# Optimization experiments

Hardware: AMD Instinct MI355X
Metric: run time of the kernel (lower is better)

## Reference

```python
import jax, jax.numpy as jnp
import numpy as np

BATCH = 2048
INPUT_DIM = 256    # == output_units, since Dense output is fed back into the cell
DEC_UNITS = 1024
OUTPUT_STEPS = 96
OUTPUT_UNITS = 256


def setup_inputs() -> dict:
    key = jax.random.key(0)
    ks = jax.random.split(key, 8)
    scale = 0.05
    return {
        "last_input": jax.random.normal(ks[0], (BATCH, INPUT_DIM), dtype=jnp.float32),
        "h0": jax.random.normal(ks[1], (BATCH, DEC_UNITS), dtype=jnp.float32),
        "c0": jax.random.normal(ks[2], (BATCH, DEC_UNITS), dtype=jnp.float32),
        # LSTMCell params (Keras layout: kernel [in, 4*units], recurrent_kernel [units, 4*units], bias [4*units]; gate order i,f,c,o)
        "Wk": jax.random.normal(ks[3], (INPUT_DIM, 4 * DEC_UNITS), dtype=jnp.float32) * scale,
        "Wr": jax.random.normal(ks[4], (DEC_UNITS, 4 * DEC_UNITS), dtype=jnp.float32) * scale,
        "b": jax.random.normal(ks[5], (4 * DEC_UNITS,), dtype=jnp.float32) * scale,
        # Dense output projection
        "Wd": jax.random.normal(ks[6], (DEC_UNITS, OUTPUT_UNITS), dtype=jnp.float32) * scale,
        "bd": jax.random.normal(ks[7], (OUTPUT_UNITS,), dtype=jnp.float32) * scale,
    }


def reference(last_input, h0, c0, Wk, Wr, b, Wd, bd):
    def step(carry, _):
        x, h, c = carry
        # fused gate GEMM: [B, in] @ [in, 4U] + [B, U] @ [U, 4U]
        z = x @ Wk + h @ Wr + b
        zi, zf, zg, zo = jnp.split(z, 4, axis=-1)  # Keras gate order: i, f, c(g), o
        i = jax.nn.sigmoid(zi)
        f = jax.nn.sigmoid(zf)
        o = jax.nn.sigmoid(zo)
        c_new = f * c + i * jnp.tanh(zg)
        h_new = o * jnp.tanh(c_new)
        pred = h_new @ Wd + bd  # fed back as next step's input
        return (pred, h_new, c_new), pred

    _, preds = jax.lax.scan(step, (last_input, h0, c0), None, length=OUTPUT_STEPS)
    # preds: [T, B, out] -> [B, T, out] (matches tf.transpose(predictions, [1,0,2]))
    return jnp.transpose(preds, (1, 0, 2))
```

## Files before the change

### kernel.cpp

```cpp
#include <hip/hip_runtime.h>
#include <hip/hip_bf16.h>
#include <stdint.h>

#define B_SZ 2048
#define U_SZ 1024
#define G_SZ 4096
#define I_SZ 256
#define O_SZ 256
#define T_SZ 96
#define K1_SZ 1280

typedef _Float16 half8 __attribute__((ext_vector_type(8)));
typedef float float4v __attribute__((ext_vector_type(4)));

__device__ inline float sigm_f(float x) { return 1.0f / (1.0f + __expf(-x)); }
__device__ inline float tanh_f(float x) { return 1.0f - 2.0f / (1.0f + __expf(2.0f * x)); }

__device__ inline short f2h(float x) {
    return __builtin_bit_cast(short, (_Float16)x);
}

__device__ inline void cp16(const void* g, void* l) {
    __builtin_amdgcn_global_load_lds(
        (const __attribute__((address_space(1))) void*)g,
        (__attribute__((address_space(3))) void*)l,
        16, 0, 0);
}


__global__ void transpose_reord(const float* __restrict__ in, float* __restrict__ out, int K) {
    __shared__ float s[32][33];
    int c0 = blockIdx.x * 32, k0 = blockIdx.y * 32;
    int tx = threadIdx.x, ty = threadIdx.y;
#pragma unroll
    for (int i = 0; i < 4; i++)
        s[ty + 8 * i][tx] = in[(long)(k0 + ty + 8 * i) * G_SZ + c0 + tx];
    __syncthreads();
#pragma unroll
    for (int i = 0; i < 4; i++) {
        int cc = ty + 8 * i;
        int c = c0 + cc;
        int n = 4 * (c & 1023) + (c >> 10);
        out[(long)n * K + k0 + tx] = s[tx][cc];
    }
}

__global__ void transpose_f32(const float* __restrict__ in, float* __restrict__ out, int R, int C) {
    __shared__ float s[32][33];
    int c0 = blockIdx.x * 32, r0 = blockIdx.y * 32;
    int tx = threadIdx.x, ty = threadIdx.y;
#pragma unroll
    for (int i = 0; i < 4; i++)
        s[ty + 8 * i][tx] = in[(long)(r0 + ty + 8 * i) * C + c0 + tx];
    __syncthreads();
#pragma unroll
    for (int i = 0; i < 4; i++)
        out[(long)(c0 + ty + 8 * i) * R + r0 + tx] = s[tx][ty + 8 * i];
}

__global__ void transpose_f16(const float* __restrict__ in, short* __restrict__ out, int R, int C) {
    __shared__ float s[32][33];
    int c0 = blockIdx.x * 32, r0 = blockIdx.y * 32;
    int tx = threadIdx.x, ty = threadIdx.y;
#pragma unroll
    for (int i = 0; i < 4; i++)
        s[ty + 8 * i][tx] = in[(long)(r0 + ty + 8 * i) * C + c0 + tx];
    __syncthreads();
#pragma unroll
    for (int i = 0; i < 4; i++)
        out[(long)(c0 + ty + 8 * i) * R + r0 + tx] = f2h(s[tx][ty + 8 * i]);
}

__global__ void cast_f16(const float* __restrict__ in, short* __restrict__ out) {
    long i = (long)blockIdx.x * 256 + threadIdx.x;
    out[i] = f2h(in[i]);
}

__global__ void build_b0t(const float* __restrict__ WkT, const float* __restrict__ WrT,
                          short* __restrict__ B0T) {
    long idx = (long)blockIdx.x * 256 + threadIdx.x;
    long n = idx / K1_SZ, k = idx % K1_SZ;
    float v = (k < I_SZ) ? WkT[n * I_SZ + k] : WrT[n * U_SZ + (k - I_SZ)];
    B0T[idx] = f2h(v);
}

__global__ void build_x0(const float* __restrict__ x0, const float* __restrict__ h0,
                         short* __restrict__ X0) {
    long idx = (long)blockIdx.x * 256 + threadIdx.x;
    long m = idx / K1_SZ, k = idx % K1_SZ;
    float v = (k < I_SZ) ? x0[m * I_SZ + k] : h0[m * U_SZ + (k - I_SZ)];
    X0[idx] = f2h(v);
}

__global__ void build_ber(const float* __restrict__ Wk, const float* __restrict__ b,
                          const float* __restrict__ bd, float* __restrict__ beR,
                          float* __restrict__ bR) {
    int c = blockIdx.x * 256 + threadIdx.x;
    float s = 0.0f;
    for (int p = 0; p < I_SZ; p++) s += bd[p] * Wk[(long)p * G_SZ + c];
    int slot = 4 * (c & 1023) + (c >> 10);
    bR[slot] = b[c];
    beR[slot] = b[c] + s;
}

__global__ void zero_ctr(unsigned int* __restrict__ c) { c[threadIdx.x] = 0u; }

__device__ __forceinline__ void gemm_core(char* smem, const char* gA, const char* gB,
                                          long Kb, int KI, int w, int l,
                                          float4v (&acc)[4][4]) {
    const int lr = l & 15, lk = l >> 4;
    const int wg = w >> 1, wb = w & 1;
    char* const lA = smem + (w * 32) * 128;
    char* const lB = smem + 32768 + (w * 16) * 128;

    auto stage = [&](int kt, int b) {
        const long go = (long)kt * 128;
        char* dA = lA + b * 49152;
        char* dB = lB + b * 49152;
#pragma unroll
        for (int ci = 0; ci < 4; ++ci) cp16(gA + (long)ci * 8 * Kb + go, dA + ci * 1024);
#pragma unroll
        for (int ci = 0; ci < 2; ++ci) cp16(gB + (long)ci * 8 * Kb + go, dB + ci * 1024);
    };
    auto compute = [&](int b) {
        const char* As = smem + b * 49152;
        const char* Bs = As + 32768;
#pragma unroll
        for (int ks = 0; ks < 2; ++ks) {
            half8 af[4], bf[4];
            const int chunk = (ks * 4 + lk) ^ (lr & 7);
#pragma unroll
            for (int mi = 0; mi < 4; ++mi)
                af[mi] = *(const half8*)(As + (wg * 64 + mi * 16 + lr) * 128 + chunk * 16);
#pragma unroll
            for (int ni = 0; ni < 4; ++ni)
                bf[ni] = *(const half8*)(Bs + (wb * 64 + ni * 16 + lr) * 128 + chunk * 16);
            __builtin_amdgcn_s_setprio(1);
#pragma unroll
            for (int mi = 0; mi < 4; ++mi)
#pragma unroll
                for (int ni = 0; ni < 4; ++ni)
                    acc[mi][ni] = __builtin_amdgcn_mfma_f32_16x16x32_f16(
                        af[mi], bf[ni], acc[mi][ni], 0, 0, 0);
            __builtin_amdgcn_s_setprio(0);
        }
    };

    stage(0, 0);
    stage(1, 1);
    int bc = 0, bs = 2;
    for (int kt = 0; kt < KI; ++kt) {
        if (kt < KI - 1)
            asm volatile("s_waitcnt vmcnt(6) lgkmcnt(0)" ::: "memory");
        else
            asm volatile("s_waitcnt vmcnt(0) lgkmcnt(0)" ::: "memory");
        __builtin_amdgcn_s_barrier();
        asm volatile("" ::: "memory");
        if (kt + 2 < KI) stage(kt + 2, bs);
        compute(bc);
        bc = (bc == 2) ? 0 : bc + 1;
        bs = (bs == 2) ? 0 : bs + 1;
    }
}

__device__ __forceinline__ void gemm_core_paced(char* smem, const char* gA, const char* gB,
                                                long Kb, int KI, int w, int l,
                                                float4v (&acc)[4][4], int tid, int xcd,
                                                unsigned int* pace, int sync_base) {
    const int lr = l & 15, lk = l >> 4;
    const int wg = w >> 1, wb = w & 1;
    char* const lA = smem + (w * 32) * 128;
    char* const lB = smem + 32768 + (w * 16) * 128;

    auto stage = [&](int kt, int b) {
        const long go = (long)kt * 128;
        char* dA = lA + b * 49152;
        char* dB = lB + b * 49152;
#pragma unroll
        for (int ci = 0; ci < 4; ++ci) cp16(gA + (long)ci * 8 * Kb + go, dA + ci * 1024);
#pragma unroll
        for (int ci = 0; ci < 2; ++ci) cp16(gB + (long)ci * 8 * Kb + go, dB + ci * 1024);
    };
    auto compute = [&](int b) {
        const char* As = smem + b * 49152;
        const char* Bs = As + 32768;
#pragma unroll
        for (int ks = 0; ks < 2; ++ks) {
            half8 af[4], bf[4];
            const int chunk = (ks * 4 + lk) ^ (lr & 7);
#pragma unroll
            for (int mi = 0; mi < 4; ++mi)
                af[mi] = *(const half8*)(As + (wg * 64 + mi * 16 + lr) * 128 + chunk * 16);
#pragma unroll
            for (int ni = 0; ni < 4; ++ni)
                bf[ni] = *(const half8*)(Bs + (wb * 64 + ni * 16 + lr) * 128 + chunk * 16);
            __builtin_amdgcn_s_setprio(1);
#pragma unroll
            for (int mi = 0; mi < 4; ++mi)
#pragma unroll
                for (int ni = 0; ni < 4; ++ni)
                    acc[mi][ni] = __builtin_amdgcn_mfma_f32_16x16x32_f16(
                        af[mi], bf[ni], acc[mi][ni], 0, 0, 0);
            __builtin_amdgcn_s_setprio(0);
        }
    };

    stage(0, 0);
    stage(1, 1);
    int bc = 0, bs = 2;
    for (int kt = 0; kt < KI; ++kt) {
        if ((kt & 3) == 0 && kt != 0) {
            asm volatile("" ::: "memory");
            if (tid == 0) {
                const unsigned int tgt = 32u * (unsigned int)(sync_base + (kt >> 2));
                __hip_atomic_fetch_add(&pace[xcd * 32], 1u, __ATOMIC_RELAXED,
                                       __HIP_MEMORY_SCOPE_AGENT);
                while (__hip_atomic_load(&pace[xcd * 32], __ATOMIC_RELAXED,
                                         __HIP_MEMORY_SCOPE_AGENT) < tgt)
                    __builtin_amdgcn_s_sleep(1);
            }
            __builtin_amdgcn_s_barrier();
            asm volatile("" ::: "memory");
        }
        if (kt < KI - 1)
            asm volatile("s_waitcnt vmcnt(6) lgkmcnt(0)" ::: "memory");
        else
            asm volatile("s_waitcnt vmcnt(0) lgkmcnt(0)" ::: "memory");
        __builtin_amdgcn_s_barrier();
        asm volatile("" ::: "memory");
        if (kt + 2 < KI) stage(kt + 2, bs);
        compute(bc);
        bc = (bc == 2) ? 0 : bc + 1;
        bs = (bs == 2) ? 0 : bs + 1;
    }
}

__global__ __launch_bounds__(512, 2) void lstm_step(
    const short* __restrict__ A, const short* __restrict__ Bm, int K,
    float* __restrict__ cT, const float* __restrict__ beR, short* __restrict__ hOut,
    unsigned int* __restrict__ pace, int sync_base) {
    __shared__ char smem[147456];

    const int tid = threadIdx.x;
    const int w = tid >> 6, l = tid & 63;
    const int wg = w >> 1, wb = w & 1;
    const int bid = blockIdx.x;
    const int xcd = bid & 7, idx = bid >> 3;
    const int n_blk = (xcd & 3) * 4 + (idx & 3);
    const int m_blk = (xcd >> 2) * 8 + (idx >> 2);
    const long Kb = (long)K * 2;

    float4v acc[4][4];
#pragma unroll
    for (int i = 0; i < 4; i++)
#pragma unroll
        for (int j = 0; j < 4; j++) acc[i][j] = (float4v)0.0f;

    const int r8 = l >> 3, s8 = l & 7, gch = s8 ^ r8;
    const char* gA = (const char*)A + ((long)(n_blk * 256 + w * 32 + r8)) * Kb + gch * 16;
    const char* gB = (const char*)Bm + ((long)(m_blk * 128 + w * 16 + r8)) * Kb + gch * 16;

    gemm_core_paced(smem, gA, gB, Kb, K >> 6, w, l, acc, tid, xcd, pace, sync_base);

    const int lr = l & 15, lk = l >> 4;
    short* hs = (short*)smem;
    __syncthreads();
    const int j_base = n_blk * 64 + wg * 16;
    const int m_base = m_blk * 128 + wb * 64;
#pragma unroll
    for (int mi = 0; mi < 4; ++mi) {
        int j = j_base + mi * 4 + lk;
        float4v bias = *(const float4v*)(beR + 4 * j);
#pragma unroll
        for (int ni = 0; ni < 4; ++ni) {
            int m = m_base + ni * 16 + lr;
            float zi = acc[mi][ni][0] + bias[0];
            float zf = acc[mi][ni][1] + bias[1];
            float zg = acc[mi][ni][2] + bias[2];
            float zo = acc[mi][ni][3] + bias[3];
            float ig = sigm_f(zi), fg = sigm_f(zf), gg = tanh_f(zg), og = sigm_f(zo);
            long cidx = (long)j * B_SZ + m;
            float cn = fg * cT[cidx] + ig * gg;
            cT[cidx] = cn;
            float h = og * tanh_f(cn);
            int mm = wb * 64 + ni * 16 + lr;
            int jj = wg * 16 + mi * 4 + lk;
            hs[mm * 64 + (jj ^ ((mm & 7) << 3))] = f2h(h);
        }
    }
    __syncthreads();
    {
        const int q = tid & 7;
        int rr = tid >> 3;
#pragma unroll
        for (int it = 0; it < 2; ++it, rr += 64) {
            uint4 v = *(const uint4*)(hs + rr * 64 + ((q ^ (rr & 7)) * 8));
            *(uint4*)(hOut + (long)(m_blk * 128 + rr) * U_SZ + n_blk * 64 + q * 8) = v;
        }
    }
}

__global__ __launch_bounds__(512, 2) void dense_out(
    const short* __restrict__ Hm, const short* __restrict__ WdT,
    const float* __restrict__ bd, float* __restrict__ out, int t_fix) {
    __shared__ char smem[147456];

    const int tid = threadIdx.x;
    const int w = tid >> 6, l = tid & 63;
    const int wg = w >> 1, wb = w & 1;
    const int o_blk = blockIdx.x, m_blk = blockIdx.y;
    const long Kb = U_SZ * 2;

    float4v acc[4][4];
#pragma unroll
    for (int i = 0; i < 4; i++)
#pragma unroll
        for (int j = 0; j < 4; j++) acc[i][j] = (float4v)0.0f;

    const int r8 = l >> 3, s8 = l & 7, gch = s8 ^ r8;
    const char* gA = (const char*)Hm + ((long)(m_blk * 256 + w * 32 + r8)) * Kb + gch * 16;
    const char* gB = (const char*)WdT + ((long)(o_blk * 128 + w * 16 + r8)) * Kb + gch * 16;

    gemm_core(smem, gA, gB, Kb, U_SZ >> 6, w, l, acc);

    const int lr = l & 15, lk = l >> 4;
#pragma unroll
    for (int ni = 0; ni < 4; ++ni) {
        int o = o_blk * 128 + wb * 64 + ni * 16 + lr;
        float bo = bd[o];
#pragma unroll
        for (int mi = 0; mi < 4; ++mi) {
#pragma unroll
            for (int r = 0; r < 4; ++r) {
                int m = m_blk * 256 + wg * 64 + mi * 16 + lk * 4 + r;
                int t = (t_fix >= 0) ? t_fix : (m >> 11);
                int b = (t_fix >= 0) ? m : (m & 2047);
                out[(long)b * (T_SZ * O_SZ) + (long)t * O_SZ + o] = acc[mi][ni][r] + bo;
            }
        }
    }
}

__global__ __launch_bounds__(512, 2) void fold_mfma(
    const short* __restrict__ WkTh, const short* __restrict__ Wdh,
    const float* __restrict__ WrT, short* __restrict__ WeT) {
    __shared__ char smem[147456];

    const int tid = threadIdx.x;
    const int w = tid >> 6, l = tid & 63;
    const int wg = w >> 1, wb = w & 1;
    const int n_blk = blockIdx.x, k_blk = blockIdx.y;
    const long Kb = I_SZ * 2;

    float4v acc[4][4];
#pragma unroll
    for (int i = 0; i < 4; i++)
#pragma unroll
        for (int j = 0; j < 4; j++) acc[i][j] = (float4v)0.0f;

    const int r8 = l >> 3, s8 = l & 7, gch = s8 ^ r8;
    const char* gA = (const char*)WkTh + ((long)(n_blk * 256 + w * 32 + r8)) * Kb + gch * 16;
    const char* gB = (const char*)Wdh + ((long)(k_blk * 128 + w * 16 + r8)) * Kb + gch * 16;

    gemm_core(smem, gA, gB, Kb, I_SZ >> 6, w, l, acc);

    const int lr = l & 15, lk = l >> 4;
#pragma unroll
    for (int mi = 0; mi < 4; ++mi)
#pragma unroll
        for (int ni = 0; ni < 4; ++ni)
#pragma unroll
            for (int r = 0; r < 4; ++r) {
                long n = n_blk * 256 + wg * 64 + mi * 16 + lk * 4 + r;
                long k = k_blk * 128 + wb * 64 + ni * 16 + lr;
                WeT[n * U_SZ + k] = f2h(WrT[n * U_SZ + k] + acc[mi][ni][r]);
            }
}

extern "C" void kernel_launch(void* const* d_in, const int* in_sizes, int n_in,
                              void* d_out, int out_size, void* d_ws, size_t ws_size,
                              hipStream_t stream) {
    (void)in_sizes; (void)n_in; (void)out_size;
    const float* x0 = (const float*)d_in[0];
    const float* h0 = (const float*)d_in[1];
    const float* c0 = (const float*)d_in[2];
    const float* Wk = (const float*)d_in[3];
    const float* Wr = (const float*)d_in[4];
    const float* bb = (const float*)d_in[5];
    const float* Wd = (const float*)d_in[6];
    const float* bd = (const float*)d_in[7];
    float* out = (float*)d_out;

    char* p = (char*)d_ws;
    auto alloc = [&](size_t bytes) {
        char* r = p;
        p += (bytes + 255) & ~(size_t)255;
        return r;
    };
    short* WeT = (short*)alloc((size_t)G_SZ * U_SZ * 2);
    short* B0T = (short*)alloc((size_t)G_SZ * K1_SZ * 2);
    short* X0 = (short*)alloc((size_t)B_SZ * K1_SZ * 2);
    short* WdT = (short*)alloc((size_t)O_SZ * U_SZ * 2);
    short* WkTh = (short*)alloc((size_t)G_SZ * I_SZ * 2);
    short* Wdh = (short*)alloc((size_t)U_SZ * I_SZ * 2);
    float* beR = (float*)alloc((size_t)U_SZ * 4 * 4);
    float* bR = (float*)alloc((size_t)U_SZ * 4 * 4);
    float* cT = (float*)alloc((size_t)U_SZ * B_SZ * 4);
    unsigned int* pace = (unsigned int*)alloc(1024);
    char* R = p;
    const size_t SLAB = (size_t)B_SZ * U_SZ * 2;
    size_t rem = (ws_size > (size_t)(R - (char*)d_ws)) ? ws_size - (size_t)(R - (char*)d_ws) : 0;
    bool hist = rem >= (size_t)T_SZ * SLAB;

    float* WkT = (float*)R;
    float* WrT = (float*)(R + (size_t)G_SZ * I_SZ * 4);

    zero_ctr<<<1, 256, 0, stream>>>(pace);
    transpose_reord<<<dim3(G_SZ / 32, I_SZ / 32), dim3(32, 8), 0, stream>>>(Wk, WkT, I_SZ);
    transpose_reord<<<dim3(G_SZ / 32, U_SZ / 32), dim3(32, 8), 0, stream>>>(Wr, WrT, U_SZ);
    cast_f16<<<(G_SZ * I_SZ) / 256, 256, 0, stream>>>(WkT, WkTh);
    cast_f16<<<(U_SZ * I_SZ) / 256, 256, 0, stream>>>(Wd, Wdh);
    fold_mfma<<<dim3(G_SZ / 256, U_SZ / 128), 512, 0, stream>>>(WkTh, Wdh, WrT, WeT);
    build_b0t<<<(int)(((size_t)G_SZ * K1_SZ) / 256), 256, 0, stream>>>(WkT, WrT, B0T);
    build_ber<<<G_SZ / 256, 256, 0, stream>>>(Wk, bb, bd, beR, bR);
    transpose_f16<<<dim3(O_SZ / 32, U_SZ / 32), dim3(32, 8), 0, stream>>>(Wd, WdT, U_SZ, O_SZ);
    transpose_f32<<<dim3(U_SZ / 32, B_SZ / 32), dim3(32, 8), 0, stream>>>(c0, cT, B_SZ, U_SZ);
    build_x0<<<(int)(((size_t)B_SZ * K1_SZ) / 256), 256, 0, stream>>>(x0, h0, X0);

    auto slab = [&](int t) -> short* {
        if (hist) return (short*)(R + (size_t)(t - 1) * SLAB);
        return (short*)(R + (size_t)((t - 1) & 1) * SLAB);
    };

    int sb = 0;
    for (int t = 1; t <= T_SZ; ++t) {
        if (t == 1) {
            lstm_step<<<256, 512, 0, stream>>>(
                B0T, X0, K1_SZ, cT, bR, slab(1), pace, sb);
            sb += ((K1_SZ >> 6) - 1) >> 2;
        } else {
            lstm_step<<<256, 512, 0, stream>>>(
                WeT, slab(t - 1), U_SZ, cT, beR, slab(t), pace, sb);
            sb += ((U_SZ >> 6) - 1) >> 2;
        }
        if (!hist)
            dense_out<<<dim3(2, B_SZ / 256), 512, 0, stream>>>(slab(t), WdT, bd, out, t - 1);
    }
    if (hist)
        dense_out<<<dim3(2, (T_SZ * B_SZ) / 256), 512, 0, stream>>>((short*)R, WdT, bd, out, -1);
}
```

Before: 3.021 ms.

## Drop per-XCD atomic pacing in LSTM step; retile dense output GEMM

Removes the cross-block atomic pacing barrier inside the LSTM step GEMM, along with its counter buffer and zeroing kernel, so blocks run unthrottled through the K loop. The dense output projection moves to a new 256-thread, double-buffered GEMM core with 128x128 tiles and a smaller LDS footprint, meant to raise occupancy and grid size. Without pacing, blocks on the same XCD may drift apart and lose the L2 reuse of shared weight tiles that the pacing was meant to keep.

```diff
diff --git a/kernel.cpp b/kernel.cpp
--- a/kernel.cpp
+++ b/kernel.cpp
@@ -102,8 +102,6 @@
     bR[slot] = b[c];
     beR[slot] = b[c] + s;
 }
-
-__global__ void zero_ctr(unsigned int* __restrict__ c) { c[threadIdx.x] = 0u; }
 
 __device__ __forceinline__ void gemm_core(char* smem, const char* gA, const char* gB,
                                           long Kb, int KI, int w, int l,
@@ -163,27 +161,26 @@
     }
 }
 
-__device__ __forceinline__ void gemm_core_paced(char* smem, const char* gA, const char* gB,
-                                                long Kb, int KI, int w, int l,
-                                                float4v (&acc)[4][4], int tid, int xcd,
-                                                unsigned int* pace, int sync_base) {
+__device__ __forceinline__ void gemm_core4(char* smem, const char* gA, const char* gB,
+                                           long Kb, int KI, int w, int l,
+                                           float4v (&acc)[4][4]) {
     const int lr = l & 15, lk = l >> 4;
     const int wg = w >> 1, wb = w & 1;
     char* const lA = smem + (w * 32) * 128;
-    char* const lB = smem + 32768 + (w * 16) * 128;
+    char* const lB = smem + 16384 + (w * 32) * 128;
 
     auto stage = [&](int kt, int b) {
         const long go = (long)kt * 128;
-        char* dA = lA + b * 49152;
-        char* dB = lB + b * 49152;
+        char* dA = lA + b * 32768;
+        char* dB = lB + b * 32768;
 #pragma unroll
         for (int ci = 0; ci < 4; ++ci) cp16(gA + (long)ci * 8 * Kb + go, dA + ci * 1024);
 #pragma unroll
-        for (int ci = 0; ci < 2; ++ci) cp16(gB + (long)ci * 8 * Kb + go, dB + ci * 1024);
+        for (int ci = 0; ci < 4; ++ci) cp16(gB + (long)ci * 8 * Kb + go, dB + ci * 1024);
     };
     auto compute = [&](int b) {
-        const char* As = smem + b * 49152;
-        const char* Bs = As + 32768;
+        const char* As = smem + b * 32768;
+        const char* Bs = As + 16384;
 #pragma unroll
         for (int ks = 0; ks < 2; ++ks) {
             half8 af[4], bf[4];
@@ -207,38 +204,23 @@
 
     stage(0, 0);
     stage(1, 1);
-    int bc = 0, bs = 2;
     for (int kt = 0; kt < KI; ++kt) {
-        if ((kt & 3) == 0 && kt != 0) {
-            asm volatile("" ::: "memory");
-            if (tid == 0) {
-                const unsigned int tgt = 32u * (unsigned int)(sync_base + (kt >> 2));
-                __hip_atomic_fetch_add(&pace[xcd * 32], 1u, __ATOMIC_RELAXED,
-                                       __HIP_MEMORY_SCOPE_AGENT);
-                while (__hip_atomic_load(&pace[xcd * 32], __ATOMIC_RELAXED,
-                                         __HIP_MEMORY_SCOPE_AGENT) < tgt)
-                    __builtin_amdgcn_s_sleep(1);
-            }
-            __builtin_amdgcn_s_barrier();
-            asm volatile("" ::: "memory");
-        }
         if (kt < KI - 1)
-            asm volatile("s_waitcnt vmcnt(6) lgkmcnt(0)" ::: "memory");
+            asm volatile("s_waitcnt vmcnt(8) lgkmcnt(0)" ::: "memory");
         else
             asm volatile("s_waitcnt vmcnt(0) lgkmcnt(0)" ::: "memory");
         __builtin_amdgcn_s_barrier();
         asm volatile("" ::: "memory");
-        if (kt + 2 < KI) stage(kt + 2, bs);
-        compute(bc);
-        bc = (bc == 2) ? 0 : bc + 1;
-        bs = (bs == 2) ? 0 : bs + 1;
+        compute(kt & 1);
+        asm volatile("" ::: "memory");
+        __builtin_amdgcn_s_barrier();
+        if (kt + 2 < KI) stage(kt + 2, kt & 1);
     }
 }
 
 __global__ __launch_bounds__(512, 2) void lstm_step(
     const short* __restrict__ A, const short* __restrict__ Bm, int K,
-    float* __restrict__ cT, const float* __restrict__ beR, short* __restrict__ hOut,
-    unsigned int* __restrict__ pace, int sync_base) {
+    float* __restrict__ cT, const float* __restrict__ beR, short* __restrict__ hOut) {
     __shared__ char smem[147456];
 
     const int tid = threadIdx.x;
@@ -260,7 +242,7 @@
     const char* gA = (const char*)A + ((long)(n_blk * 256 + w * 32 + r8)) * Kb + gch * 16;
     const char* gB = (const char*)Bm + ((long)(m_blk * 128 + w * 16 + r8)) * Kb + gch * 16;
 
-    gemm_core_paced(smem, gA, gB, Kb, K >> 6, w, l, acc, tid, xcd, pace, sync_base);
+    gemm_core(smem, gA, gB, Kb, K >> 6, w, l, acc);
 
     const int lr = l & 15, lk = l >> 4;
     short* hs = (short*)smem;
@@ -300,10 +282,10 @@
     }
 }
 
-__global__ __launch_bounds__(512, 2) void dense_out(
+__global__ __launch_bounds__(256, 2) void dense_out(
     const short* __restrict__ Hm, const short* __restrict__ WdT,
     const float* __restrict__ bd, float* __restrict__ out, int t_fix) {
-    __shared__ char smem[147456];
+    __shared__ char smem[65536];
 
     const int tid = threadIdx.x;
     const int w = tid >> 6, l = tid & 63;
@@ -318,10 +300,10 @@
         for (int j = 0; j < 4; j++) acc[i][j] = (float4v)0.0f;
 
     const int r8 = l >> 3, s8 = l & 7, gch = s8 ^ r8;
-    const char* gA = (const char*)Hm + ((long)(m_blk * 256 + w * 32 + r8)) * Kb + gch * 16;
-    const char* gB = (const char*)WdT + ((long)(o_blk * 128 + w * 16 + r8)) * Kb + gch * 16;
-
-    gemm_core(smem, gA, gB, Kb, U_SZ >> 6, w, l, acc);
+    const char* gA = (const char*)Hm + ((long)(m_blk * 128 + w * 32 + r8)) * Kb + gch * 16;
+    const char* gB = (const char*)WdT + ((long)(o_blk * 128 + w * 32 + r8)) * Kb + gch * 16;
+
+    gemm_core4(smem, gA, gB, Kb, U_SZ >> 6, w, l, acc);
 
     const int lr = l & 15, lk = l >> 4;
 #pragma unroll
@@ -332,7 +314,7 @@
         for (int mi = 0; mi < 4; ++mi) {
 #pragma unroll
             for (int r = 0; r < 4; ++r) {
-                int m = m_blk * 256 + wg * 64 + mi * 16 + lk * 4 + r;
+                int m = m_blk * 128 + wg * 64 + mi * 16 + lk * 4 + r;
                 int t = (t_fix >= 0) ? t_fix : (m >> 11);
                 int b = (t_fix >= 0) ? m : (m & 2047);
                 out[(long)b * (T_SZ * O_SZ) + (long)t * O_SZ + o] = acc[mi][ni][r] + bo;
@@ -406,7 +388,6 @@
     float* beR = (float*)alloc((size_t)U_SZ * 4 * 4);
     float* bR = (float*)alloc((size_t)U_SZ * 4 * 4);
     float* cT = (float*)alloc((size_t)U_SZ * B_SZ * 4);
-    unsigned int* pace = (unsigned int*)alloc(1024);
     char* R = p;
     const size_t SLAB = (size_t)B_SZ * U_SZ * 2;
     size_t rem = (ws_size > (size_t)(R - (char*)d_ws)) ? ws_size - (size_t)(R - (char*)d_ws) : 0;
@@ -415,7 +396,6 @@
     float* WkT = (float*)R;
     float* WrT = (float*)(R + (size_t)G_SZ * I_SZ * 4);
 
-    zero_ctr<<<1, 256, 0, stream>>>(pace);
     transpose_reord<<<dim3(G_SZ / 32, I_SZ / 32), dim3(32, 8), 0, stream>>>(Wk, WkT, I_SZ);
     transpose_reord<<<dim3(G_SZ / 32, U_SZ / 32), dim3(32, 8), 0, stream>>>(Wr, WrT, U_SZ);
     cast_f16<<<(G_SZ * I_SZ) / 256, 256, 0, stream>>>(WkT, WkTh);
@@ -432,20 +412,14 @@
         return (short*)(R + (size_t)((t - 1) & 1) * SLAB);
     };
 
-    int sb = 0;
     for (int t = 1; t <= T_SZ; ++t) {
-        if (t == 1) {
-            lstm_step<<<256, 512, 0, stream>>>(
-                B0T, X0, K1_SZ, cT, bR, slab(1), pace, sb);
-            sb += ((K1_SZ >> 6) - 1) >> 2;
-        } else {
-            lstm_step<<<256, 512, 0, stream>>>(
-                WeT, slab(t - 1), U_SZ, cT, beR, slab(t), pace, sb);
-            sb += ((U_SZ >> 6) - 1) >> 2;
-        }
+        if (t == 1)
+            lstm_step<<<256, 512, 0, stream>>>(B0T, X0, K1_SZ, cT, bR, slab(1));
+        else
+            lstm_step<<<256, 512, 0, stream>>>(WeT, slab(t - 1), U_SZ, cT, beR, slab(t));
         if (!hist)
-            dense_out<<<dim3(2, B_SZ / 256), 512, 0, stream>>>(slab(t), WdT, bd, out, t - 1);
+            dense_out<<<dim3(2, B_SZ / 128), 256, 0, stream>>>(slab(t), WdT, bd, out, t - 1);
     }
     if (hist)
-        dense_out<<<dim3(2, (T_SZ * B_SZ) / 256), 512, 0, stream>>>((short*)R, WdT, bd, out, -1);
-}
+        dense_out<<<dim3(2, (T_SZ * B_SZ) / 128), 256, 0, stream>>>((short*)R, WdT, bd, out, -1);
+}
```

Result: faster. 2.826 ms (-6.4%).
